# Performance work log

Measured on AMD Instinct MI355X. Metric: run time of the kernel, lower is better.

The kernel has to match this reference:

```python
import jax, jax.numpy as jnp
import numpy as np
from jax import lax

EPS = 1e-5
DN = ('NCHW', 'OIHW', 'NCHW')

def conv3x3(x, w, stride=1):
    return lax.conv_general_dilated(x, w, window_strides=(stride, stride),
                                    padding=((1, 1), (1, 1)), dimension_numbers=DN)

def batchnorm(x, gamma, beta, mean, var):
    # inference-mode BN, per-channel (NCHW)
    inv = gamma / jnp.sqrt(var + EPS)
    return x * inv[None, :, None, None] + (beta - mean * inv)[None, :, None, None]

def per_elem_act(x, codes):
    # codes: int array of length C*H*W; one activation id per flattened element
    # 0=relu, 1=identity, 2=tanh, 3=sigmoid  (stands in for SAFS per-element search space)
    c = codes.reshape((1,) + x.shape[1:])
    return jnp.where(c == 0, jax.nn.relu(x),
           jnp.where(c == 1, x,
           jnp.where(c == 2, jnp.tanh(x), jax.nn.sigmoid(x))))

def setup_inputs() -> dict:
    key = jax.random.key(0)
    ks = jax.random.split(key, 6)
    B, C, H, W = 32, 64, 112, 112
    x = jax.random.normal(ks[0], (B, C, H, W), jnp.float32)
    conv1_w = jax.random.normal(ks[1], (C, C, 3, 3), jnp.float32) * 0.05
    conv2_w = jax.random.normal(ks[2], (C, C, 3, 3), jnp.float32) * 0.05
    nelem = C * H * W
    return {
        'x': x, 'conv1_w': conv1_w, 'conv2_w': conv2_w,
        'gamma1': jnp.ones((C,), jnp.float32), 'beta1': jnp.zeros((C,), jnp.float32),
        'mean1': jnp.zeros((C,), jnp.float32), 'var1': jnp.ones((C,), jnp.float32),
        'gamma2': jnp.ones((C,), jnp.float32), 'beta2': jnp.zeros((C,), jnp.float32),
        'mean2': jnp.zeros((C,), jnp.float32), 'var2': jnp.ones((C,), jnp.float32),
        'act_codes_feat': jax.random.randint(ks[3], (nelem,), 0, 4, jnp.int32),
        'act_codes_sc': jax.random.randint(ks[4], (nelem,), 0, 4, jnp.int32),
    }

def reference(x, conv1_w, conv2_w, gamma1, beta1, mean1, var1,
              gamma2, beta2, mean2, var2, act_codes_feat, act_codes_sc):
    # features: conv3x3 -> BN -> per-element activation -> conv3x3 -> BN
    h = conv3x3(x, conv1_w, stride=1)
    h = batchnorm(h, gamma1, beta1, mean1, var1)
    h = per_elem_act(h, act_codes_feat)
    h = conv3x3(h, conv2_w, stride=1)
    h = batchnorm(h, gamma2, beta2, mean2, var2)
    # shortcut (stride==1, in_planes==planes): just per-element activation of x
    out = h + per_elem_act(x, act_codes_sc)
    return out
```

## Files before the change

kernel.cpp:

```cpp
#include <hip/hip_runtime.h>
#include <math.h>

#define BB 32
#define CC 64
#define HH 112
#define WW 112
#define HW 12544

typedef __bf16  bf16x8 __attribute__((ext_vector_type(8)));
typedef float   f32x4  __attribute__((ext_vector_type(4)));
typedef int     int4v  __attribute__((ext_vector_type(4)));
typedef unsigned short ushort4v __attribute__((ext_vector_type(4)));

constexpr float EPSV = 1e-5f;

__device__ __forceinline__ unsigned short bf16bits(float f) {
    __bf16 b = (__bf16)f;
    return __builtin_bit_cast(unsigned short, b);
}

__device__ __forceinline__ float apply_act(float v, int code) {
    float e2 = __expf(2.f * v);
    float th = 1.f - 2.f / (e2 + 1.f);
    float sg = 1.f / (1.f + __expf(-v));
    float r = fmaxf(v, 0.f);
    r = (code == 1) ? v  : r;
    r = (code == 2) ? th : r;
    r = (code == 3) ? sg : r;
    return r;
}

__global__ __launch_bounds__(256)
void prepack_w(const float* __restrict__ w1, const float* __restrict__ w2,
               unsigned short* __restrict__ wpk)
{
    int idx  = blockIdx.x * 256 + threadIdx.x;
    int conv = idx / 36864;
    int r    = idx % 36864;
    int step = r >> 9;
    int e    = r & 511;
    int l    = e >> 3;
    int j    = e & 7;
    int mt   = step & 3;
    int ti   = step >> 2;
    int tap  = ti % 9;
    int icch = ti / 9;
    int oc   = mt * 16 + (l & 15);
    int ic   = icch * 32 + (l >> 4) * 8 + j;
    const float* w = conv ? w2 : w1;
    wpk[idx] = bf16bits(w[(oc * 64 + ic) * 9 + tap]);
}

__global__ __launch_bounds__(256)
void x_to_nhwc(const float* __restrict__ x, unsigned short* __restrict__ xo, int n0)
{
    int t   = threadIdx.x;
    int px  = blockIdx.x * 64 + (t >> 2);
    int nl  = blockIdx.y;
    int icq = t & 3;
    const float* src = x + ((size_t)(n0 + nl) * CC + icq * 16) * HW + px;
    ushort4v p[4];
    #pragma unroll
    for (int q = 0; q < 4; ++q)
        #pragma unroll
        for (int j = 0; j < 4; ++j)
            p[q][j] = bf16bits(src[(q * 4 + j) * HW]);
    unsigned short* dst = xo + ((size_t)nl * HW + px) * CC + icq * 16;
    *(int4v*)(dst)     = ((int4v*)p)[0];
    *(int4v*)(dst + 8) = ((int4v*)p)[1];
}

__global__ __launch_bounds__(256)
void codes_to_nhwc(const int* __restrict__ ci, int* __restrict__ co)
{
    int t   = threadIdx.x;
    int px  = blockIdx.x * 64 + (t >> 2);
    int icq = t & 3;
    const int* src = ci + icq * 16 * HW + px;
    int4v p[4];
    #pragma unroll
    for (int q = 0; q < 4; ++q)
        #pragma unroll
        for (int j = 0; j < 4; ++j)
            p[q][j] = src[(q * 4 + j) * HW];
    int* dst = co + (size_t)px * CC + icq * 16;
    #pragma unroll
    for (int q = 0; q < 4; ++q) *(int4v*)(dst + q * 4) = p[q];
}

template<bool FIRST>
__global__ __launch_bounds__(256, 3)
void conv_mfma(const unsigned short* __restrict__ in_nhwc,
               const unsigned short* __restrict__ wpk,
               const float* __restrict__ gamma, const float* __restrict__ beta,
               const float* __restrict__ mean,  const float* __restrict__ var,
               const int*   __restrict__ codes_t,
               const int*   __restrict__ codes_sc,
               const float* __restrict__ x0,
               unsigned short* __restrict__ hout,
               float* __restrict__ out,
               int nof)
{
    __shared__ char smem[41472];
    const int t    = threadIdx.x;
    const int lane = t & 63, wv = t >> 6;
    const int l15  = lane & 15, l4 = lane >> 4;
    const int tile = blockIdx.x, n = blockIdx.y;
    const int ty0  = (tile / 7) * 16, tx0 = (tile % 7) * 16;

    int gofs[6]; bool inb[6];
    #pragma unroll
    for (int i = 0; i < 6; ++i) {
        int c = t + i * 256;
        int px = c >> 2, slot = c & 3;
        int ry = px / 18, rx = px % 18;
        int gy = ty0 + ry - 1, gx = tx0 + rx - 1;
        inb[i] = (c < 1296) && ((unsigned)gy < (unsigned)HH) && ((unsigned)gx < (unsigned)WW);
        int slotp = slot ^ ((px >> 1) & 3);
        gofs[i] = (((n * HH + gy) * WW + gx) * CC + slotp * 8) * 2;
    }

    int baddr[6][3];
    #pragma unroll
    for (int row = 0; row < 6; ++row)
        #pragma unroll
        for (int kx = 0; kx < 3; ++kx) {
            int px = (wv * 4 + row) * 18 + l15 + kx;
            baddr[row][kx] = px * 64 + ((l4 ^ ((px >> 1) & 3)) << 4);
        }

    const char* wb = (const char*)wpk + lane * 16;

    #pragma unroll
    for (int i = 0; i < 6; ++i) {
        if (i < 5 || t < 16) {
            int4v v = {0, 0, 0, 0};
            if (inb[i]) v = *(const int4v*)((const char*)in_nhwc + gofs[i]);
            *(int4v*)(smem + (t + i * 256) * 16) = v;
        }
    }
    __syncthreads();

    int4v hold[6];
    #pragma unroll
    for (int i = 0; i < 6; ++i) {
        int4v v = {0, 0, 0, 0};
        if (inb[i]) v = *(const int4v*)((const char*)in_nhwc + gofs[i] + 64);
        hold[i] = v;
    }

    f32x4 acc[4][4];
    #pragma unroll
    for (int mt = 0; mt < 4; ++mt)
        #pragma unroll
        for (int r = 0; r < 4; ++r) acc[mt][r] = (f32x4){0.f, 0.f, 0.f, 0.f};

    #pragma unroll
    for (int s = 0; s < 18; ++s) {
        const int icch = s / 9, tap = s % 9, ky = tap / 3, kx = tap % 3;
        bf16x8 a[4];
        #pragma unroll
        for (int mt = 0; mt < 4; ++mt)
            a[mt] = *(const bf16x8*)(wb + (s * 4 + mt) * 1024);
        bf16x8 b[4];
        #pragma unroll
        for (int r = 0; r < 4; ++r)
            b[r] = *(const bf16x8*)(smem + baddr[r + ky][kx] + icch * 20736);
        #pragma unroll
        for (int r = 0; r < 4; ++r)
            #pragma unroll
            for (int mt = 0; mt < 4; ++mt)
                acc[mt][r] = __builtin_amdgcn_mfma_f32_16x16x32_bf16(a[mt], b[r], acc[mt][r], 0, 0, 0);
        if (s == 8) {
            #pragma unroll
            for (int i = 0; i < 6; ++i)
                if (i < 5 || t < 16)
                    *(int4v*)(smem + 20736 + (t + i * 256) * 16) = hold[i];
            __syncthreads();
        }
    }

    float sc[4][4], sh[4][4];
    #pragma unroll
    for (int mt = 0; mt < 4; ++mt)
        #pragma unroll
        for (int g = 0; g < 4; ++g) {
            int oc = mt * 16 + l4 * 4 + g;
            float s0 = gamma[oc] * rsqrtf(var[oc] + EPSV);
            sc[mt][g] = s0;
            sh[mt][g] = beta[oc] - mean[oc] * s0;
        }

    if (FIRST) {
        #pragma unroll
        for (int r = 0; r < 4; ++r) {
            int py = ty0 + wv * 4 + r, px = tx0 + l15;
            size_t pbase = ((size_t)(n + nof) * HW + py * WW + px) * CC;
            const int* ct = codes_t + (py * WW + px) * CC;
            #pragma unroll
            for (int mt = 0; mt < 4; ++mt) {
                int4v cd = *(const int4v*)(ct + mt * 16 + l4 * 4);
                ushort4v pk;
                #pragma unroll
                for (int g = 0; g < 4; ++g) {
                    float v = acc[mt][r][g] * sc[mt][g] + sh[mt][g];
                    pk[g] = bf16bits(apply_act(v, cd[g]));
                }
                *(ushort4v*)(hout + pbase + mt * 16 + l4 * 4) = pk;
            }
        }
    } else {
        #pragma unroll
        for (int r = 0; r < 4; ++r) {
            int py = ty0 + wv * 4 + r, px = tx0 + l15;
            #pragma unroll
            for (int mt = 0; mt < 4; ++mt) {
                #pragma unroll
                for (int g = 0; g < 4; ++g) {
                    int oc = mt * 16 + l4 * 4 + g;
                    size_t oidx = ((size_t)n * CC + oc) * HW + py * WW + px;
                    int code = codes_sc[oc * HW + py * WW + px];
                    float v = acc[mt][r][g] * sc[mt][g] + sh[mt][g];
                    out[oidx] = v + apply_act(x0[oidx], code);
                }
            }
        }
    }
}

extern "C" void kernel_launch(void* const* d_in, const int* in_sizes, int n_in,
                              void* d_out, int out_size, void* d_ws, size_t ws_size,
                              hipStream_t stream) {
    const float* x        = (const float*)d_in[0];
    const float* conv1_w  = (const float*)d_in[1];
    const float* conv2_w  = (const float*)d_in[2];
    const float* gamma1   = (const float*)d_in[3];
    const float* beta1    = (const float*)d_in[4];
    const float* mean1    = (const float*)d_in[5];
    const float* var1     = (const float*)d_in[6];
    const float* gamma2   = (const float*)d_in[7];
    const float* beta2    = (const float*)d_in[8];
    const float* mean2    = (const float*)d_in[9];
    const float* var2     = (const float*)d_in[10];
    const int*   codes_f  = (const int*)d_in[11];
    const int*   codes_sc = (const int*)d_in[12];
    float* out = (float*)d_out;

    unsigned short* h    = (unsigned short*)d_ws;
    unsigned short* xbf  = (unsigned short*)((char*)d_ws + 51380224);
    int*            ctns = (int*)((char*)d_ws + 77070336);
    unsigned short* wpk  = (unsigned short*)((char*)d_ws + 80281600);

    prepack_w<<<288, 256, 0, stream>>>(conv1_w, conv2_w, wpk);
    codes_to_nhwc<<<196, 256, 0, stream>>>(codes_f, ctns);

    for (int g = 0; g < 2; ++g) {
        int n0 = g * 16;
        x_to_nhwc<<<dim3(196, 16), 256, 0, stream>>>(x, xbf, n0);
        conv_mfma<true><<<dim3(49, 16), 256, 0, stream>>>(
            xbf, wpk, gamma1, beta1, mean1, var1, ctns, nullptr, nullptr,
            h, nullptr, n0);
    }
    conv_mfma<false><<<dim3(49, BB), 256, 0, stream>>>(
        h, wpk + 36864, gamma2, beta2, mean2, var2, nullptr, codes_sc, x,
        nullptr, out, 0);
}
```

Baseline: 493.1 us.

## Compress activation codes to bytes, remap blocks per XCD, prefetch weights

Activation codes for both the feature and shortcut paths are converted once into byte arrays, which cuts their read traffic in the conv epilogues by four. The conv grid is flattened and remapped so that neighbouring tiles of the same image land on the same XCD, which should improve L2 reuse of the halo rows. Weight fragments for the next step are loaded into registers one iteration early, so their latency overlaps the MFMA work. This raises register pressure and adds one extra preprocessing kernel launch.

```diff
diff --git a/kernel.cpp b/kernel.cpp
--- a/kernel.cpp
+++ b/kernel.cpp
@@ -71,21 +71,27 @@
 }
 
 __global__ __launch_bounds__(256)
-void codes_to_nhwc(const int* __restrict__ ci, int* __restrict__ co)
-{
-    int t   = threadIdx.x;
-    int px  = blockIdx.x * 64 + (t >> 2);
-    int icq = t & 3;
-    const int* src = ci + icq * 16 * HW + px;
-    int4v p[4];
-    #pragma unroll
-    for (int q = 0; q < 4; ++q)
-        #pragma unroll
-        for (int j = 0; j < 4; ++j)
-            p[q][j] = src[(q * 4 + j) * HW];
-    int* dst = co + (size_t)px * CC + icq * 16;
-    #pragma unroll
-    for (int q = 0; q < 4; ++q) *(int4v*)(dst + q * 4) = p[q];
+void codes_to_bytes_nhwc(const int* __restrict__ ci, unsigned char* __restrict__ co)
+{
+    int idx  = blockIdx.x * 256 + threadIdx.x;
+    int px   = idx / 16;
+    int quad = idx % 16;
+    unsigned char b[4];
+    #pragma unroll
+    for (int j = 0; j < 4; ++j)
+        b[j] = (unsigned char)ci[(quad * 4 + j) * HW + px];
+    *(unsigned int*)(co + (size_t)px * CC + quad * 4) = *(unsigned int*)b;
+}
+
+__global__ __launch_bounds__(256)
+void codes_to_bytes_nchw(const int* __restrict__ ci, unsigned char* __restrict__ co)
+{
+    int idx = blockIdx.x * 256 + threadIdx.x;
+    int4v v = *(const int4v*)(ci + idx * 4);
+    unsigned char b[4];
+    #pragma unroll
+    for (int j = 0; j < 4; ++j) b[j] = (unsigned char)v[j];
+    *(unsigned int*)(co + idx * 4) = *(unsigned int*)b;
 }
 
 template<bool FIRST>
@@ -94,8 +100,8 @@
                const unsigned short* __restrict__ wpk,
                const float* __restrict__ gamma, const float* __restrict__ beta,
                const float* __restrict__ mean,  const float* __restrict__ var,
-               const int*   __restrict__ codes_t,
-               const int*   __restrict__ codes_sc,
+               const unsigned char* __restrict__ cbt,
+               const unsigned char* __restrict__ cbs,
                const float* __restrict__ x0,
                unsigned short* __restrict__ hout,
                float* __restrict__ out,
@@ -105,8 +111,15 @@
     const int t    = threadIdx.x;
     const int lane = t & 63, wv = t >> 6;
     const int l15  = lane & 15, l4 = lane >> 4;
-    const int tile = blockIdx.x, n = blockIdx.y;
-    const int ty0  = (tile / 7) * 16, tx0 = (tile % 7) * 16;
+
+    const int bid   = blockIdx.x;
+    const int xcd   = bid & 7;
+    const int q     = bid >> 3;
+    const int strip = xcd + 8 * (q / 7);
+    const int j7    = q % 7;
+    const int ty    = strip % 7;
+    const int n     = strip / 7;
+    const int ty0   = ty * 16, tx0 = j7 * 16;
 
     int gofs[6]; bool inb[6];
     #pragma unroll
@@ -139,6 +152,9 @@
             *(int4v*)(smem + (t + i * 256) * 16) = v;
         }
     }
+    bf16x8 a_cur[4], a_nxt[4];
+    #pragma unroll
+    for (int mt = 0; mt < 4; ++mt) a_cur[mt] = *(const bf16x8*)(wb + mt * 1024);
     __syncthreads();
 
     int4v hold[6];
@@ -158,10 +174,11 @@
     #pragma unroll
     for (int s = 0; s < 18; ++s) {
         const int icch = s / 9, tap = s % 9, ky = tap / 3, kx = tap % 3;
-        bf16x8 a[4];
-        #pragma unroll
-        for (int mt = 0; mt < 4; ++mt)
-            a[mt] = *(const bf16x8*)(wb + (s * 4 + mt) * 1024);
+        if (s < 17) {
+            #pragma unroll
+            for (int mt = 0; mt < 4; ++mt)
+                a_nxt[mt] = *(const bf16x8*)(wb + ((s + 1) * 4 + mt) * 1024);
+        }
         bf16x8 b[4];
         #pragma unroll
         for (int r = 0; r < 4; ++r)
@@ -170,7 +187,7 @@
         for (int r = 0; r < 4; ++r)
             #pragma unroll
             for (int mt = 0; mt < 4; ++mt)
-                acc[mt][r] = __builtin_amdgcn_mfma_f32_16x16x32_bf16(a[mt], b[r], acc[mt][r], 0, 0, 0);
+                acc[mt][r] = __builtin_amdgcn_mfma_f32_16x16x32_bf16(a_cur[mt], b[r], acc[mt][r], 0, 0, 0);
         if (s == 8) {
             #pragma unroll
             for (int i = 0; i < 6; ++i)
@@ -178,6 +195,8 @@
                     *(int4v*)(smem + 20736 + (t + i * 256) * 16) = hold[i];
             __syncthreads();
         }
+        #pragma unroll
+        for (int mt = 0; mt < 4; ++mt) a_cur[mt] = a_nxt[mt];
     }
 
     float sc[4][4], sh[4][4];
@@ -196,15 +215,15 @@
         for (int r = 0; r < 4; ++r) {
             int py = ty0 + wv * 4 + r, px = tx0 + l15;
             size_t pbase = ((size_t)(n + nof) * HW + py * WW + px) * CC;
-            const int* ct = codes_t + (py * WW + px) * CC;
+            const unsigned char* ct = cbt + ((size_t)py * WW + px) * CC;
             #pragma unroll
             for (int mt = 0; mt < 4; ++mt) {
-                int4v cd = *(const int4v*)(ct + mt * 16 + l4 * 4);
+                unsigned int cd4 = *(const unsigned int*)(ct + mt * 16 + l4 * 4);
                 ushort4v pk;
                 #pragma unroll
                 for (int g = 0; g < 4; ++g) {
                     float v = acc[mt][r][g] * sc[mt][g] + sh[mt][g];
-                    pk[g] = bf16bits(apply_act(v, cd[g]));
+                    pk[g] = bf16bits(apply_act(v, (int)((cd4 >> (8 * g)) & 255u)));
                 }
                 *(ushort4v*)(hout + pbase + mt * 16 + l4 * 4) = pk;
             }
@@ -219,7 +238,7 @@
                 for (int g = 0; g < 4; ++g) {
                     int oc = mt * 16 + l4 * 4 + g;
                     size_t oidx = ((size_t)n * CC + oc) * HW + py * WW + px;
-                    int code = codes_sc[oc * HW + py * WW + px];
+                    int code = (int)cbs[oc * HW + py * WW + px];
                     float v = acc[mt][r][g] * sc[mt][g] + sh[mt][g];
                     out[oidx] = v + apply_act(x0[oidx], code);
                 }
@@ -248,20 +267,22 @@
 
     unsigned short* h    = (unsigned short*)d_ws;
     unsigned short* xbf  = (unsigned short*)((char*)d_ws + 51380224);
-    int*            ctns = (int*)((char*)d_ws + 77070336);
-    unsigned short* wpk  = (unsigned short*)((char*)d_ws + 80281600);
+    unsigned short* wpk  = (unsigned short*)((char*)d_ws + 77070336);
+    unsigned char*  cbt  = (unsigned char*)((char*)d_ws + 77217792);
+    unsigned char*  cbs  = (unsigned char*)((char*)d_ws + 78020608);
 
     prepack_w<<<288, 256, 0, stream>>>(conv1_w, conv2_w, wpk);
-    codes_to_nhwc<<<196, 256, 0, stream>>>(codes_f, ctns);
+    codes_to_bytes_nhwc<<<784, 256, 0, stream>>>(codes_f, cbt);
+    codes_to_bytes_nchw<<<784, 256, 0, stream>>>(codes_sc, cbs);
 
     for (int g = 0; g < 2; ++g) {
         int n0 = g * 16;
         x_to_nhwc<<<dim3(196, 16), 256, 0, stream>>>(x, xbf, n0);
-        conv_mfma<true><<<dim3(49, 16), 256, 0, stream>>>(
-            xbf, wpk, gamma1, beta1, mean1, var1, ctns, nullptr, nullptr,
+        conv_mfma<true><<<784, 256, 0, stream>>>(
+            xbf, wpk, gamma1, beta1, mean1, var1, cbt, nullptr, nullptr,
             h, nullptr, n0);
     }
-    conv_mfma<false><<<dim3(49, BB), 256, 0, stream>>>(
-        h, wpk + 36864, gamma2, beta2, mean2, var2, nullptr, codes_sc, x,
+    conv_mfma<false><<<1568, 256, 0, stream>>>(
+        h, wpk + 36864, gamma2, beta2, mean2, var2, nullptr, cbs, x,
         nullptr, out, 0);
 }
```

New measurement: 472.0 us. -4.3%, faster.
